# Optimization experiments

Measured on AMD Instinct MI355X. Metric: run time of the kernel, lower is better.

## Reference

```python
import jax, jax.numpy as jnp
import numpy as np

B, C, H, W = 4, 192, 56, 56
D_STATE, D_CONV, EXPAND = 16, 3, 2
D_INNER = EXPAND * C
DT_RANK = (C + 15) // 16  # 12


def setup_inputs() -> dict:
    key = jax.random.key(0)
    ks = jax.random.split(key, 16)
    s = 0.02
    return {
        "x": jax.random.normal(ks[0], (B, C, H, W), jnp.float32),
        "ln1_g": jnp.ones((C,), jnp.float32),
        "ln1_b": jnp.zeros((C,), jnp.float32),
        "in_proj_w": jax.random.normal(ks[1], (2 * D_INNER, C), jnp.float32) * s,
        "conv1d_w": jax.random.normal(ks[2], (D_INNER, 1, D_CONV), jnp.float32) * s,
        "conv1d_b": jnp.zeros((D_INNER,), jnp.float32),
        "x_proj_w": jax.random.normal(ks[3], (DT_RANK + 2 * D_STATE, D_INNER), jnp.float32) * s,
        "dt_proj_w": jax.random.normal(ks[4], (D_INNER, DT_RANK), jnp.float32) * (DT_RANK ** -0.5),
        "dt_proj_b": jax.random.uniform(ks[5], (D_INNER,), jnp.float32, -4.6, -2.3),
        "A_log": jnp.tile(jnp.log(jnp.arange(1, D_STATE + 1, dtype=jnp.float32)), (D_INNER, 1)),
        "Dskip": jnp.ones((D_INNER,), jnp.float32),
        "out_proj_w": jax.random.normal(ks[6], (C, D_INNER), jnp.float32) * s,
        "dw_w": jax.random.normal(ks[7], (C, 1, 3, 3), jnp.float32) * s,
        "bn_g": jnp.ones((C,), jnp.float32),
        "bn_b": jnp.zeros((C,), jnp.float32),
        "bn_mean": jax.random.normal(ks[8], (C,), jnp.float32) * 0.1,
        "bn_var": jax.random.uniform(ks[9], (C,), jnp.float32, 0.5, 1.5),
        "ln2_g": jnp.ones((C,), jnp.float32),
        "ln2_b": jnp.zeros((C,), jnp.float32),
        "mlp_w1": jax.random.normal(ks[10], (4 * C, C), jnp.float32) * s,
        "mlp_b1": jnp.zeros((4 * C,), jnp.float32),
        "mlp_w2": jax.random.normal(ks[11], (C, 4 * C), jnp.float32) * s,
        "mlp_b2": jnp.zeros((C,), jnp.float32),
    }


def _ln(x, g, b, eps=1e-5):
    m = jnp.mean(x, -1, keepdims=True)
    v = jnp.var(x, -1, keepdims=True)
    return (x - m) * jax.lax.rsqrt(v + eps) * g + b


def _gelu(x):
    return jax.nn.gelu(x, approximate=False)


def _mamba(xf, in_proj_w, conv1d_w, conv1d_b, x_proj_w, dt_proj_w, dt_proj_b, A_log, Dskip, out_proj_w):
    # xf: (B, L, C) tokens
    Bn, L, _ = xf.shape
    xz = jnp.einsum('blc,ec->ble', xf, in_proj_w)  # (B, L, 2*d_inner)
    xm, z = jnp.split(xz, 2, axis=-1)
    # causal depthwise conv1d over L
    xm_t = jnp.transpose(xm, (0, 2, 1))  # (B, d_inner, L)
    conv = jax.lax.conv_general_dilated(
        xm_t, conv1d_w, (1,), [(D_CONV - 1, 0)],
        feature_group_count=D_INNER,
        dimension_numbers=('NCH', 'OIH', 'NCH'))
    xm = jax.nn.silu(jnp.transpose(conv + conv1d_b[None, :, None], (0, 2, 1)))  # (B, L, d_inner)
    x_dbl = jnp.einsum('bld,ed->ble', xm, x_proj_w)
    dt = x_dbl[..., :DT_RANK]
    Bm = x_dbl[..., DT_RANK:DT_RANK + D_STATE]   # (B, L, n)
    Cm = x_dbl[..., DT_RANK + D_STATE:]          # (B, L, n)
    delta = jax.nn.softplus(jnp.einsum('blr,dr->bld', dt, dt_proj_w) + dt_proj_b)
    A = -jnp.exp(A_log)                           # (d_inner, n)
    deltaA = jnp.exp(delta[..., None] * A)        # (B, L, d, n)
    deltaBx = (delta * xm)[..., None] * Bm[:, :, None, :]  # (B, L, d, n)

    def step(h, inp):
        dA, dBx, Ct = inp
        h = dA * h + dBx                          # (B, d, n)
        y = jnp.einsum('bdn,bn->bd', h, Ct)
        return h, y

    h0 = jnp.zeros((Bn, D_INNER, D_STATE), xm.dtype)
    _, ys = jax.lax.scan(step, h0, (jnp.transpose(deltaA, (1, 0, 2, 3)),
                                    jnp.transpose(deltaBx, (1, 0, 2, 3)),
                                    jnp.transpose(Cm, (1, 0, 2))))
    y = jnp.transpose(ys, (1, 0, 2)) + xm * Dskip  # (B, L, d_inner)
    y = y * jax.nn.silu(z)
    return jnp.einsum('bld,cd->blc', y, out_proj_w)


def reference(x, ln1_g, ln1_b, in_proj_w, conv1d_w, conv1d_b, x_proj_w, dt_proj_w, dt_proj_b,
              A_log, Dskip, out_proj_w, dw_w, bn_g, bn_b, bn_mean, bn_var,
              ln2_g, ln2_b, mlp_w1, mlp_b1, mlp_w2, mlp_b2):
    Bn, Cn, Hn, Wn = x.shape
    # --- branch 1: LN -> SS2D (Mamba over flattened tokens) + skip
    t = jnp.transpose(x, (0, 2, 3, 1))            # (B, H, W, C)
    t = _ln(t, ln1_g, ln1_b)
    tokens = t.reshape(Bn, Hn * Wn, Cn)           # row-major = rearrange 'b c h w -> b (h w) c' after LN
    y = _mamba(tokens, in_proj_w, conv1d_w, conv1d_b, x_proj_w, dt_proj_w, dt_proj_b,
               A_log, Dskip, out_proj_w)
    x1 = x + jnp.transpose(y.reshape(Bn, Hn, Wn, Cn), (0, 3, 1, 2))
    # --- branch 2: depthwise conv -> BN(eval) -> GELU + skip
    dw = jax.lax.conv_general_dilated(x1, dw_w, (1, 1), [(1, 1), (1, 1)],
                                      feature_group_count=Cn,
                                      dimension_numbers=('NCHW', 'OIHW', 'NCHW'))
    bn = (dw - bn_mean[None, :, None, None]) * jax.lax.rsqrt(bn_var + 1e-5)[None, :, None, None]
    bn = bn * bn_g[None, :, None, None] + bn_b[None, :, None, None]
    x2 = x1 + _gelu(bn)
    # --- branch 3: LN -> MLP + skip
    t = jnp.transpose(x2, (0, 2, 3, 1))
    t = _ln(t, ln2_g, ln2_b)
    h = _gelu(jnp.einsum('bhwc,ec->bhwe', t, mlp_w1) + mlp_b1)
    m = jnp.einsum('bhwe,ce->bhwc', h, mlp_w2) + mlp_b2
    return x2 + jnp.transpose(m, (0, 3, 1, 2))
```

## Files before the change

kernel.cpp:

```cpp
#include <hip/hip_runtime.h>
#include <hip/hip_bf16.h>
#include <math.h>

#define BATCH 4
#define CCH   192
#define HH    56
#define WW    56
#define LSEQ  (HH*WW)
#define NTOK  (BATCH*LSEQ)
#define DST   16
#define DIN   384
#define DTR   12
#define XDM   (DTR + 2*DST)
#define CL    32
#define NC    (LSEQ/CL)

typedef __attribute__((ext_vector_type(8))) short short8;
typedef __attribute__((ext_vector_type(4))) short short4v;
typedef __attribute__((ext_vector_type(4))) float floatx4;

__device__ __forceinline__ float siluf(float x)  { return x / (1.f + __expf(-x)); }
__device__ __forceinline__ float geluf(float x)  { return 0.5f * x * (1.f + erff(x * 0.70710678118654752f)); }
__device__ __forceinline__ float softplusf(float x) { return (x > 20.f) ? x : log1pf(__expf(x)); }
__device__ __forceinline__ float bf2f(short u) {
    union { unsigned int i; float f; } cv; cv.i = ((unsigned int)(unsigned short)u) << 16; return cv.f;
}
__device__ __forceinline__ short f2bf_bits(float v) {
    __hip_bfloat16 h = __float2bfloat16(v);
    return *(short*)&h;
}

#define WSZ0 147456
#define WSZ1 16896
#define WSZ2 73728
#define WSZ3 147456
#define WSZ4 147456
__global__ __launch_bounds__(256) void cvt_weights(const float* __restrict__ w0, const float* __restrict__ w1,
                                                   const float* __restrict__ w2, const float* __restrict__ w3,
                                                   const float* __restrict__ w4,
                                                   __hip_bfloat16* __restrict__ o0, __hip_bfloat16* __restrict__ o1,
                                                   __hip_bfloat16* __restrict__ o2, __hip_bfloat16* __restrict__ o3,
                                                   __hip_bfloat16* __restrict__ o4) {
    int i = blockIdx.x * 256 + threadIdx.x;
    if (i < WSZ0) { o0[i] = __float2bfloat16(w0[i]); return; } i -= WSZ0;
    if (i < WSZ1) { o1[i] = __float2bfloat16(w1[i]); return; } i -= WSZ1;
    if (i < WSZ2) { o2[i] = __float2bfloat16(w2[i]); return; } i -= WSZ2;
    if (i < WSZ3) { o3[i] = __float2bfloat16(w3[i]); return; } i -= WSZ3;
    if (i < WSZ4) { o4[i] = __float2bfloat16(w4[i]); }
}

__global__ __launch_bounds__(256) void ln_kernel(const float* __restrict__ x,
                                                 const float* __restrict__ g,
                                                 const float* __restrict__ bta,
                                                 __hip_bfloat16* __restrict__ out) {
    __shared__ float tile[CCH * 65];
    __shared__ float gs[CCH], bs[CCH];
    int t = threadIdx.x;
    int b = blockIdx.y, hw0 = blockIdx.x * 64;
    const float* xb = x + (size_t)b * CCH * LSEQ + hw0;
#pragma unroll 8
    for (int k = 0; k < 48; k++) {
        int idx = k * 256 + t;
        int c = idx >> 6, w = idx & 63;
        tile[c * 65 + w] = xb[(size_t)c * LSEQ + w];
    }
    if (t < CCH) { gs[t] = g[t]; bs[t] = bta[t]; }
    __syncthreads();
    int lane = t & 63, wave = t >> 6;
    int tk = lane & 15, p = lane >> 4;
    int tok = wave * 16 + tk;
    float s = 0.f, s2 = 0.f;
#pragma unroll 8
    for (int i = 0; i < 48; i++) {
        float v = tile[(p * 48 + i) * 65 + tok];
        s += v; s2 += v * v;
    }
    s += __shfl_xor(s, 16); s2 += __shfl_xor(s2, 16);
    s += __shfl_xor(s, 32); s2 += __shfl_xor(s2, 32);
    float mean = s * (1.f / CCH);
    float rstd = rsqrtf(s2 * (1.f / CCH) - mean * mean + 1e-5f);
    int j = lane >> 2, q = lane & 3;
    float mj = __shfl(mean, j);
    float rj = __shfl(rstd, j);
    int wtok = wave * 16 + j;
    __hip_bfloat16* op = out + (size_t)(b * LSEQ + hw0 + wtok) * CCH + q * 48;
#pragma unroll
    for (int kk = 0; kk < 6; kk++) {
        short8 pk;
#pragma unroll
        for (int e = 0; e < 8; e++) {
            int c = q * 48 + kk * 8 + e;
            float v = (tile[c * 65 + wtok] - mj) * rj * gs[c] + bs[c];
            pk[e] = f2bf_bits(v);
        }
        *(short8*)(op + kk * 8) = pk;
    }
}

template<int EPI, typename OutT>
__global__ __launch_bounds__(256) void gemm_mfma(const __hip_bfloat16* __restrict__ A,
                                                 const __hip_bfloat16* __restrict__ W,
                                                 const float* __restrict__ bias,
                                                 const float* __restrict__ res,
                                                 OutT* __restrict__ Cout,
                                                 int N, int K) {
    __shared__ __align__(16) __hip_bfloat16 As[128 * 40];
    __shared__ __align__(16) __hip_bfloat16 Bs[128 * 40];
    int tid = threadIdx.x;
    int bm = blockIdx.y * 128, bn = blockIdx.x * 128;
    int wave = tid >> 6, lane = tid & 63;
    int wm = (wave >> 1) * 64, wn = (wave & 1) * 64;
    int lm = lane & 15, quad = lane >> 4;
    floatx4 acc[4][4] = {};
    int lrow = tid >> 2;
    int lcol = (tid & 3) * 8;
    for (int k0 = 0; k0 < K; k0 += 32) {
#pragma unroll
        for (int p = 0; p < 2; p++) {
            int row = lrow + p * 64;
            *(short8*)&As[row * 40 + lcol] = *(const short8*)(A + (size_t)(bm + row) * K + k0 + lcol);
            int n = bn + row;
            short8 bv = {0,0,0,0,0,0,0,0};
            if (n < N) bv = *(const short8*)(W + (size_t)n * K + k0 + lcol);
            *(short8*)&Bs[row * 40 + lcol] = bv;
        }
        __syncthreads();
        short8 a[4], b[4];
#pragma unroll
        for (int i = 0; i < 4; i++) a[i] = *(const short8*)&As[(wm + i * 16 + lm) * 40 + quad * 8];
#pragma unroll
        for (int j = 0; j < 4; j++) b[j] = *(const short8*)&Bs[(wn + j * 16 + lm) * 40 + quad * 8];
#pragma unroll
        for (int i = 0; i < 4; i++)
#pragma unroll
            for (int j = 0; j < 4; j++)
                acc[i][j] = __builtin_amdgcn_mfma_f32_16x16x32_bf16(a[i], b[j], acc[i][j], 0, 0, 0);
        __syncthreads();
    }
#pragma unroll
    for (int j = 0; j < 4; j++) {
        int n = bn + wn + j * 16 + lm;
        if (n >= N) continue;
        float bv = (EPI == 2 || EPI == 4) ? bias[n] : 0.f;
#pragma unroll
        for (int i = 0; i < 4; i++) {
            int mrow = bm + wm + i * 16 + quad * 4;
            if (EPI == 3 || EPI == 4) {
                int bb = mrow / LSEQ;
                int l0 = mrow % LSEQ;
                size_t oidx = ((size_t)(bb * CCH + n)) * LSEQ + l0;
                float4 xr = *(const float4*)(res + oidx);
                float4 v;
                v.x = acc[i][j][0] + bv + xr.x;
                v.y = acc[i][j][1] + bv + xr.y;
                v.z = acc[i][j][2] + bv + xr.z;
                v.w = acc[i][j][3] + bv + xr.w;
                *(float4*)((float*)Cout + oidx) = v;
            } else {
#pragma unroll
                for (int r = 0; r < 4; r++) {
                    float v = acc[i][j][r];
                    if (EPI == 2) { v += bv; v = geluf(v); }
                    Cout[(size_t)(mrow + r) * N + n] = (OutT)v;
                }
            }
        }
    }
}

__global__ __launch_bounds__(256) void gemm_nt_dt(const float* __restrict__ A,
                                                  const float* __restrict__ Wt,
                                                  const float* __restrict__ bias,
                                                  float* __restrict__ Cout) {
    __shared__ float As[16][64 + 1];
    __shared__ float Ws[16][64 + 1];
    const int N = DIN, K = DTR;
    int tid = threadIdx.x;
    int bm = blockIdx.y * 64;
    int bn = blockIdx.x * 64;
    int lr = tid >> 4;
    int lk = tid & 15;
    int tm = (tid >> 4) << 2;
    int tn = (tid & 15) << 2;
    float acc[4][4] = {};
#pragma unroll
    for (int p = 0; p < 4; p++) {
        int m = bm + lr + 16 * p;
        As[lk][lr + 16 * p] = (lk < K) ? A[(size_t)m * XDM + lk] : 0.f;
        int n = bn + lr + 16 * p;
        Ws[lk][lr + 16 * p] = (lk < K) ? Wt[(size_t)n * K + lk] : 0.f;
    }
    __syncthreads();
#pragma unroll
    for (int kk = 0; kk < 12; kk++) {
        float a[4], w[4];
#pragma unroll
        for (int i = 0; i < 4; i++) a[i] = As[kk][tm + i];
#pragma unroll
        for (int j = 0; j < 4; j++) w[j] = Ws[kk][tn + j];
#pragma unroll
        for (int i = 0; i < 4; i++)
#pragma unroll
            for (int j = 0; j < 4; j++)
                acc[i][j] += a[i] * w[j];
    }
#pragma unroll
    for (int i = 0; i < 4; i++) {
        int m = bm + tm + i;
#pragma unroll
        for (int j = 0; j < 4; j++) {
            int n = bn + tn + j;
            Cout[(size_t)m * N + n] = softplusf(acc[i][j] + bias[n]);
        }
    }
}

__global__ __launch_bounds__(256) void conv1d_silu(const __hip_bfloat16* __restrict__ xz,
                                                   const float* __restrict__ w,
                                                   const float* __restrict__ bias,
                                                   float* __restrict__ out,
                                                   __hip_bfloat16* __restrict__ out_bf) {
    int idx = blockIdx.x * 256 + threadIdx.x;
    if (idx >= NTOK * (DIN / 4)) return;
    int m = idx / (DIN / 4), d = (idx % (DIN / 4)) * 4;
    int l = m % LSEQ;
    short4v cur = *(const short4v*)&xz[(size_t)m * (2 * DIN) + d];
    short4v p1 = {0,0,0,0}, p2 = {0,0,0,0};
    if (l >= 1) p1 = *(const short4v*)&xz[(size_t)(m - 1) * (2 * DIN) + d];
    if (l >= 2) p2 = *(const short4v*)&xz[(size_t)(m - 2) * (2 * DIN) + d];
    float4 bv = *(const float4*)&bias[d];
    float ob[4];
    float4 of;
#pragma unroll
    for (int jj = 0; jj < 4; jj++) {
        float w0 = w[(d + jj) * 3 + 0], w1 = w[(d + jj) * 3 + 1], w2 = w[(d + jj) * 3 + 2];
        float acc = ((const float*)&bv)[jj] + w2 * bf2f(cur[jj]) + w1 * bf2f(p1[jj]) + w0 * bf2f(p2[jj]);
        float v = siluf(acc);
        ((float*)&of)[jj] = v;
        ob[jj] = v;
    }
    *(float4*)&out[(size_t)m * DIN + d] = of;
    short4v obv = { f2bf_bits(ob[0]), f2bf_bits(ob[1]), f2bf_bits(ob[2]), f2bf_bits(ob[3]) };
    *(short4v*)&out_bf[(size_t)m * DIN + d] = obv;
}

__global__ __launch_bounds__(256) void scan_phase1(const float* __restrict__ delta,
                                                   const float* __restrict__ xm,
                                                   const float* __restrict__ xdbl,
                                                   const float* __restrict__ A_log,
                                                   float* __restrict__ Pbuf,
                                                   float* __restrict__ Qbuf) {
    __shared__ float b_s[CL][16];
    int t = threadIdx.x;
    int b = blockIdx.z, c = blockIdx.x, d0 = blockIdx.y * 128;
    int m0 = b * LSEQ + c * CL;
    {
        int i = t >> 3, q = (t & 7) * 2;
        *(float2*)&b_s[i][q] = *(const float2*)&xdbl[(size_t)(m0 + i) * XDM + DTR + q];
    }
    __syncthreads();
    int d = d0 + (t >> 1), half = t & 1;
    float An[8];
#pragma unroll
    for (int n4 = 0; n4 < 2; n4++) {
        float4 a = *(const float4*)&A_log[d * DST + half * 8 + n4 * 4];
        An[n4 * 4 + 0] = -__expf(a.x);
        An[n4 * 4 + 1] = -__expf(a.y);
        An[n4 * 4 + 2] = -__expf(a.z);
        An[n4 * 4 + 3] = -__expf(a.w);
    }
    float Q[8];
#pragma unroll
    for (int n = 0; n < 8; n++) Q[n] = 0.f;
    float s = 0.f;
    const float* dp = delta + (size_t)m0 * DIN + d;
    const float* xp = xm    + (size_t)m0 * DIN + d;
#pragma unroll 4
    for (int i = 0; i < CL; i++) {
        float dlt = dp[(size_t)i * DIN];
        float xv  = xp[(size_t)i * DIN];
        s += dlt;
        float tt = dlt * xv;
#pragma unroll
        for (int n = 0; n < 8; n++) {
            float dA = __expf(dlt * An[n]);
            Q[n] = dA * Q[n] + tt * b_s[i][half * 8 + n];
        }
    }
    size_t o = ((size_t)(b * NC + c) * DIN + d) * DST + half * 8;
#pragma unroll
    for (int n4 = 0; n4 < 2; n4++) {
        float4 Pv, Qv;
        Pv.x = __expf(An[n4 * 4 + 0] * s);
        Pv.y = __expf(An[n4 * 4 + 1] * s);
        Pv.z = __expf(An[n4 * 4 + 2] * s);
        Pv.w = __expf(An[n4 * 4 + 3] * s);
        Qv.x = Q[n4 * 4 + 0]; Qv.y = Q[n4 * 4 + 1];
        Qv.z = Q[n4 * 4 + 2]; Qv.w = Q[n4 * 4 + 3];
        *(float4*)&Pbuf[o + n4 * 4] = Pv;
        *(float4*)&Qbuf[o + n4 * 4] = Qv;
    }
}

__global__ __launch_bounds__(256) void scan_phase2(const float* __restrict__ Pbuf,
                                                   const float* __restrict__ Qbuf,
                                                   float* __restrict__ Hin) {
    int t = blockIdx.x * 256 + threadIdx.x;
    if (t >= BATCH * DIN * DST) return;
    int b = t / (DIN * DST);
    int rem = t % (DIN * DST);
    float h = 0.f;
#pragma unroll 7
    for (int c = 0; c < NC; c++) {
        size_t o = (size_t)(b * NC + c) * (DIN * DST) + rem;
        Hin[o] = h;
        h = Pbuf[o] * h + Qbuf[o];
    }
}

__global__ __launch_bounds__(256) void scan_phase3(const float* __restrict__ delta,
                                                   const float* __restrict__ xm,
                                                   const float* __restrict__ xdbl,
                                                   const __hip_bfloat16* __restrict__ xz,
                                                   const float* __restrict__ A_log,
                                                   const float* __restrict__ Dskip,
                                                   const float* __restrict__ Hin,
                                                   __hip_bfloat16* __restrict__ ybuf) {
    __shared__ float bc_s[CL][32];
    int t = threadIdx.x;
    int b = blockIdx.z, c = blockIdx.x, d0 = blockIdx.y * 128;
    int m0 = b * LSEQ + c * CL;
    {
        int i = t >> 3, q = (t & 7) * 4;
        *(float4*)&bc_s[i][q] = *(const float4*)&xdbl[(size_t)(m0 + i) * XDM + DTR + q];
    }
    __syncthreads();
    int d = d0 + (t >> 1), half = t & 1;
    float An[8];
#pragma unroll
    for (int n4 = 0; n4 < 2; n4++) {
        float4 a = *(const float4*)&A_log[d * DST + half * 8 + n4 * 4];
        An[n4 * 4 + 0] = -__expf(a.x);
        An[n4 * 4 + 1] = -__expf(a.y);
        An[n4 * 4 + 2] = -__expf(a.z);
        An[n4 * 4 + 3] = -__expf(a.w);
    }
    float h[8];
    size_t o = ((size_t)(b * NC + c) * DIN + d) * DST + half * 8;
    {
        float4 h0 = *(const float4*)&Hin[o];
        float4 h1 = *(const float4*)&Hin[o + 4];
        h[0] = h0.x; h[1] = h0.y; h[2] = h0.z; h[3] = h0.w;
        h[4] = h1.x; h[5] = h1.y; h[6] = h1.z; h[7] = h1.w;
    }
    float Dv = Dskip[d];
    const float* dp = delta + (size_t)m0 * DIN + d;
    const float* xp = xm    + (size_t)m0 * DIN + d;
    const __hip_bfloat16* zp = xz + (size_t)m0 * (2 * DIN) + DIN + d;
    __hip_bfloat16* yo = ybuf + (size_t)m0 * DIN + d;
#pragma unroll 2
    for (int i = 0; i < CL; i++) {
        float dlt = dp[(size_t)i * DIN];
        float xv  = xp[(size_t)i * DIN];
        float tt = dlt * xv;
        float y = 0.f;
#pragma unroll
        for (int n = 0; n < 8; n++) {
            float dA = __expf(dlt * An[n]);
            h[n] = dA * h[n] + tt * bc_s[i][half * 8 + n];
            y += h[n] * bc_s[i][16 + half * 8 + n];
        }
        y += __shfl_xor(y, 1);
        if (half == 0) {
            float zv = bf2f(*(const short*)(zp + (size_t)i * (2 * DIN)));
            yo[(size_t)i * DIN] = __float2bfloat16((y + xv * Dv) * siluf(zv));
        }
    }
}

__global__ __launch_bounds__(256) void dwconv_bn_gelu(const float* __restrict__ x1,
                                                      const float* __restrict__ wdw,
                                                      const float* __restrict__ bn_g,
                                                      const float* __restrict__ bn_b,
                                                      const float* __restrict__ bn_mean,
                                                      const float* __restrict__ bn_var,
                                                      float* __restrict__ x2) {
    int idx = blockIdx.x * 256 + threadIdx.x;
    if (idx >= NTOK * CCH) return;
    int w = idx % WW; int tmp = idx / WW;
    int h = tmp % HH; tmp /= HH;
    int c = tmp % CCH; int b = tmp / CCH;
    const float* base = x1 + ((size_t)(b * CCH + c)) * LSEQ;
    float acc = 0.f;
#pragma unroll
    for (int dh = -1; dh <= 1; dh++) {
        int hh = h + dh;
        if (hh < 0 || hh >= HH) continue;
#pragma unroll
        for (int dw = -1; dw <= 1; dw++) {
            int wcol = w + dw;
            if (wcol < 0 || wcol >= WW) continue;
            acc += wdw[c * 9 + (dh + 1) * 3 + (dw + 1)] * base[hh * WW + wcol];
        }
    }
    float bn = (acc - bn_mean[c]) * rsqrtf(bn_var[c] + 1e-5f) * bn_g[c] + bn_b[c];
    x2[idx] = x1[idx] + geluf(bn);
}

extern "C" void kernel_launch(void* const* d_in, const int* in_sizes, int n_in,
                              void* d_out, int out_size, void* d_ws, size_t ws_size,
                              hipStream_t stream) {
    const float* x         = (const float*)d_in[0];
    const float* ln1_g     = (const float*)d_in[1];
    const float* ln1_b     = (const float*)d_in[2];
    const float* in_proj_w = (const float*)d_in[3];
    const float* conv_w    = (const float*)d_in[4];
    const float* conv_b    = (const float*)d_in[5];
    const float* x_proj_w  = (const float*)d_in[6];
    const float* dt_proj_w = (const float*)d_in[7];
    const float* dt_proj_b = (const float*)d_in[8];
    const float* A_log     = (const float*)d_in[9];
    const float* Dskip     = (const float*)d_in[10];
    const float* out_proj_w= (const float*)d_in[11];
    const float* dw_w      = (const float*)d_in[12];
    const float* bn_g      = (const float*)d_in[13];
    const float* bn_b      = (const float*)d_in[14];
    const float* bn_mean   = (const float*)d_in[15];
    const float* bn_var    = (const float*)d_in[16];
    const float* ln2_g     = (const float*)d_in[17];
    const float* ln2_b     = (const float*)d_in[18];
    const float* mlp_w1    = (const float*)d_in[19];
    const float* mlp_b1    = (const float*)d_in[20];
    const float* mlp_w2    = (const float*)d_in[21];
    const float* mlp_b2    = (const float*)d_in[22];
    float* out = (float*)d_out;

    float* ws = (float*)d_ws;
    __hip_bfloat16* xz_bf = (__hip_bfloat16*)ws;
    float* xm_act = (float*)(xz_bf + (size_t)NTOK * 768);
    float* deltab = xm_act + (size_t)NTOK * DIN;
    float* xdbl   = deltab + (size_t)NTOK * DIN;
    float* mo     = xdbl   + (size_t)NTOK * XDM;
    float* x1     = mo     + (size_t)NTOK * CCH;
    float* x2     = x1     + (size_t)NTOK * CCH;
    __hip_bfloat16* tokens_bf = (__hip_bfloat16*)(x2 + (size_t)NTOK * CCH);
    __hip_bfloat16* xm_bf     = tokens_bf + (size_t)NTOK * CCH;
    __hip_bfloat16* ybuf_bf   = xm_bf + (size_t)NTOK * DIN;
    __hip_bfloat16* wpool     = ybuf_bf + (size_t)NTOK * DIN;
    __hip_bfloat16* in_w_bf   = wpool;
    __hip_bfloat16* xp_w_bf   = in_w_bf + WSZ0;
    __hip_bfloat16* op_w_bf   = xp_w_bf + WSZ1;
    __hip_bfloat16* w1_bf     = op_w_bf + WSZ2;
    __hip_bfloat16* w2_bf     = w1_bf + WSZ3;
    float* Pbuf = mo;
    float* Qbuf = x1;
    float* Hin  = x2;
    __hip_bfloat16* hidden_bf = (__hip_bfloat16*)deltab;

    cvt_weights<<<(WSZ0 + WSZ1 + WSZ2 + WSZ3 + WSZ4 + 255) / 256, 256, 0, stream>>>(
        in_proj_w, x_proj_w, out_proj_w, mlp_w1, mlp_w2,
        in_w_bf, xp_w_bf, op_w_bf, w1_bf, w2_bf);
    ln_kernel<<<dim3(LSEQ / 64, BATCH), 256, 0, stream>>>(x, ln1_g, ln1_b, tokens_bf);
    gemm_mfma<0, __hip_bfloat16><<<dim3(768 / 128, NTOK / 128), 256, 0, stream>>>(tokens_bf, in_w_bf, nullptr, nullptr, xz_bf, 768, CCH);
    conv1d_silu<<<(NTOK * (DIN / 4) + 255) / 256, 256, 0, stream>>>(xz_bf, conv_w, conv_b, xm_act, xm_bf);
    gemm_mfma<0, float><<<dim3(1, NTOK / 128), 256, 0, stream>>>(xm_bf, xp_w_bf, nullptr, nullptr, xdbl, XDM, DIN);
    gemm_nt_dt<<<dim3(DIN / 64, NTOK / 64), 256, 0, stream>>>(xdbl, dt_proj_w, dt_proj_b, deltab);
    scan_phase1<<<dim3(NC, DIN / 128, BATCH), 256, 0, stream>>>(deltab, xm_act, xdbl, A_log, Pbuf, Qbuf);
    scan_phase2<<<(BATCH * DIN * DST + 255) / 256, 256, 0, stream>>>(Pbuf, Qbuf, Hin);
    scan_phase3<<<dim3(NC, DIN / 128, BATCH), 256, 0, stream>>>(deltab, xm_act, xdbl, xz_bf, A_log, Dskip, Hin, ybuf_bf);
    gemm_mfma<3, float><<<dim3(2, NTOK / 128), 256, 0, stream>>>(ybuf_bf, op_w_bf, nullptr, x, x1, CCH, DIN);
    dwconv_bn_gelu<<<(NTOK * CCH + 255) / 256, 256, 0, stream>>>(x1, dw_w, bn_g, bn_b, bn_mean, bn_var, x2);
    ln_kernel<<<dim3(LSEQ / 64, BATCH), 256, 0, stream>>>(x2, ln2_g, ln2_b, tokens_bf);
    gemm_mfma<2, __hip_bfloat16><<<dim3(768 / 128, NTOK / 128), 256, 0, stream>>>(tokens_bf, w1_bf, mlp_b1, nullptr, hidden_bf, 768, CCH);
    gemm_mfma<4, float><<<dim3(2, NTOK / 128), 256, 0, stream>>>(hidden_bf, w2_bf, mlp_b2, x2, out, CCH, 4 * CCH);
}
```

Before: 321.6 us.

## Fold dt_proj into x_proj GEMM, store scan inputs in bf16, vectorize dwconv

Precomputes a combined 416x384 weight (dt_proj_w @ x_proj_w[:12] stacked with the B/C rows), so one MFMA GEMM produces softplus(delta) in bf16 plus B/C in fp32. This removes the separate fp32 x_proj output and the small dt GEMM kernel. The scan kernels now read delta and the conv output as bf16, halving their traffic, and the fp32 copy of the conv output is dropped. The depthwise conv now handles four outputs per thread with float4 loads. The price is extra bf16 rounding on delta and the scan input, which may reduce accuracy.

```diff
diff --git a/kernel.cpp b/kernel.cpp
--- a/kernel.cpp
+++ b/kernel.cpp
@@ -12,6 +12,7 @@
 #define DIN   384
 #define DTR   12
 #define XDM   (DTR + 2*DST)
+#define NXC   416
 #define CL    32
 #define NC    (LSEQ/CL)
 
@@ -31,22 +32,37 @@
 }
 
 #define WSZ0 147456
-#define WSZ1 16896
 #define WSZ2 73728
 #define WSZ3 147456
 #define WSZ4 147456
-__global__ __launch_bounds__(256) void cvt_weights(const float* __restrict__ w0, const float* __restrict__ w1,
+__global__ __launch_bounds__(256) void cvt_weights(const float* __restrict__ w0,
                                                    const float* __restrict__ w2, const float* __restrict__ w3,
                                                    const float* __restrict__ w4,
-                                                   __hip_bfloat16* __restrict__ o0, __hip_bfloat16* __restrict__ o1,
+                                                   __hip_bfloat16* __restrict__ o0,
                                                    __hip_bfloat16* __restrict__ o2, __hip_bfloat16* __restrict__ o3,
                                                    __hip_bfloat16* __restrict__ o4) {
     int i = blockIdx.x * 256 + threadIdx.x;
     if (i < WSZ0) { o0[i] = __float2bfloat16(w0[i]); return; } i -= WSZ0;
-    if (i < WSZ1) { o1[i] = __float2bfloat16(w1[i]); return; } i -= WSZ1;
     if (i < WSZ2) { o2[i] = __float2bfloat16(w2[i]); return; } i -= WSZ2;
     if (i < WSZ3) { o3[i] = __float2bfloat16(w3[i]); return; } i -= WSZ3;
     if (i < WSZ4) { o4[i] = __float2bfloat16(w4[i]); }
+}
+
+__global__ __launch_bounds__(256) void make_wcomb(const float* __restrict__ xp_w,
+                                                  const float* __restrict__ dt_w,
+                                                  __hip_bfloat16* __restrict__ wcomb) {
+    int i = blockIdx.x * 256 + threadIdx.x;
+    if (i >= NXC * DIN) return;
+    int row = i / DIN, k = i % DIN;
+    float v;
+    if (row < DIN) {
+        v = 0.f;
+#pragma unroll
+        for (int r = 0; r < DTR; r++) v += dt_w[row * DTR + r] * xp_w[r * DIN + k];
+    } else {
+        v = xp_w[(row - DIN + DTR) * DIN + k];
+    }
+    wcomb[i] = __float2bfloat16(v);
 }
 
 __global__ __launch_bounds__(256) void ln_kernel(const float* __restrict__ x,
@@ -103,6 +119,7 @@
                                                  const float* __restrict__ bias,
                                                  const float* __restrict__ res,
                                                  OutT* __restrict__ Cout,
+                                                 float* __restrict__ aux,
                                                  int N, int K) {
     __shared__ __align__(16) __hip_bfloat16 As[128 * 40];
     __shared__ __align__(16) __hip_bfloat16 Bs[128 * 40];
@@ -141,6 +158,24 @@
     for (int j = 0; j < 4; j++) {
         int n = bn + wn + j * 16 + lm;
         if (n >= N) continue;
+        if (EPI == 5) {
+#pragma unroll
+            for (int i = 0; i < 4; i++) {
+                int mrow = bm + wm + i * 16 + quad * 4;
+                if (n < DIN) {
+                    float bv = bias[n];
+#pragma unroll
+                    for (int r = 0; r < 4; r++)
+                        Cout[(size_t)(mrow + r) * DIN + n] = (OutT)softplusf(acc[i][j][r] + bv);
+                } else {
+                    int nb = n - DIN;
+#pragma unroll
+                    for (int r = 0; r < 4; r++)
+                        aux[(size_t)(mrow + r) * 32 + nb] = acc[i][j][r];
+                }
+            }
+            continue;
+        }
         float bv = (EPI == 2 || EPI == 4) ? bias[n] : 0.f;
 #pragma unroll
         for (int i = 0; i < 4; i++) {
@@ -168,57 +203,9 @@
     }
 }
 
-__global__ __launch_bounds__(256) void gemm_nt_dt(const float* __restrict__ A,
-                                                  const float* __restrict__ Wt,
-                                                  const float* __restrict__ bias,
-                                                  float* __restrict__ Cout) {
-    __shared__ float As[16][64 + 1];
-    __shared__ float Ws[16][64 + 1];
-    const int N = DIN, K = DTR;
-    int tid = threadIdx.x;
-    int bm = blockIdx.y * 64;
-    int bn = blockIdx.x * 64;
-    int lr = tid >> 4;
-    int lk = tid & 15;
-    int tm = (tid >> 4) << 2;
-    int tn = (tid & 15) << 2;
-    float acc[4][4] = {};
-#pragma unroll
-    for (int p = 0; p < 4; p++) {
-        int m = bm + lr + 16 * p;
-        As[lk][lr + 16 * p] = (lk < K) ? A[(size_t)m * XDM + lk] : 0.f;
-        int n = bn + lr + 16 * p;
-        Ws[lk][lr + 16 * p] = (lk < K) ? Wt[(size_t)n * K + lk] : 0.f;
-    }
-    __syncthreads();
-#pragma unroll
-    for (int kk = 0; kk < 12; kk++) {
-        float a[4], w[4];
-#pragma unroll
-        for (int i = 0; i < 4; i++) a[i] = As[kk][tm + i];
-#pragma unroll
-        for (int j = 0; j < 4; j++) w[j] = Ws[kk][tn + j];
-#pragma unroll
-        for (int i = 0; i < 4; i++)
-#pragma unroll
-            for (int j = 0; j < 4; j++)
-                acc[i][j] += a[i] * w[j];
-    }
-#pragma unroll
-    for (int i = 0; i < 4; i++) {
-        int m = bm + tm + i;
-#pragma unroll
-        for (int j = 0; j < 4; j++) {
-            int n = bn + tn + j;
-            Cout[(size_t)m * N + n] = softplusf(acc[i][j] + bias[n]);
-        }
-    }
-}
-
 __global__ __launch_bounds__(256) void conv1d_silu(const __hip_bfloat16* __restrict__ xz,
                                                    const float* __restrict__ w,
                                                    const float* __restrict__ bias,
-                                                   float* __restrict__ out,
                                                    __hip_bfloat16* __restrict__ out_bf) {
     int idx = blockIdx.x * 256 + threadIdx.x;
     if (idx >= NTOK * (DIN / 4)) return;
@@ -229,24 +216,19 @@
     if (l >= 1) p1 = *(const short4v*)&xz[(size_t)(m - 1) * (2 * DIN) + d];
     if (l >= 2) p2 = *(const short4v*)&xz[(size_t)(m - 2) * (2 * DIN) + d];
     float4 bv = *(const float4*)&bias[d];
-    float ob[4];
-    float4 of;
+    short4v obv;
 #pragma unroll
     for (int jj = 0; jj < 4; jj++) {
         float w0 = w[(d + jj) * 3 + 0], w1 = w[(d + jj) * 3 + 1], w2 = w[(d + jj) * 3 + 2];
         float acc = ((const float*)&bv)[jj] + w2 * bf2f(cur[jj]) + w1 * bf2f(p1[jj]) + w0 * bf2f(p2[jj]);
-        float v = siluf(acc);
-        ((float*)&of)[jj] = v;
-        ob[jj] = v;
-    }
-    *(float4*)&out[(size_t)m * DIN + d] = of;
-    short4v obv = { f2bf_bits(ob[0]), f2bf_bits(ob[1]), f2bf_bits(ob[2]), f2bf_bits(ob[3]) };
+        obv[jj] = f2bf_bits(siluf(acc));
+    }
     *(short4v*)&out_bf[(size_t)m * DIN + d] = obv;
 }
 
-__global__ __launch_bounds__(256) void scan_phase1(const float* __restrict__ delta,
-                                                   const float* __restrict__ xm,
-                                                   const float* __restrict__ xdbl,
+__global__ __launch_bounds__(256) void scan_phase1(const __hip_bfloat16* __restrict__ delta,
+                                                   const __hip_bfloat16* __restrict__ xm,
+                                                   const float* __restrict__ bc,
                                                    const float* __restrict__ A_log,
                                                    float* __restrict__ Pbuf,
                                                    float* __restrict__ Qbuf) {
@@ -256,7 +238,7 @@
     int m0 = b * LSEQ + c * CL;
     {
         int i = t >> 3, q = (t & 7) * 2;
-        *(float2*)&b_s[i][q] = *(const float2*)&xdbl[(size_t)(m0 + i) * XDM + DTR + q];
+        *(float2*)&b_s[i][q] = *(const float2*)&bc[(size_t)(m0 + i) * 32 + q];
     }
     __syncthreads();
     int d = d0 + (t >> 1), half = t & 1;
@@ -273,12 +255,12 @@
 #pragma unroll
     for (int n = 0; n < 8; n++) Q[n] = 0.f;
     float s = 0.f;
-    const float* dp = delta + (size_t)m0 * DIN + d;
-    const float* xp = xm    + (size_t)m0 * DIN + d;
+    const __hip_bfloat16* dp = delta + (size_t)m0 * DIN + d;
+    const __hip_bfloat16* xp = xm    + (size_t)m0 * DIN + d;
 #pragma unroll 4
     for (int i = 0; i < CL; i++) {
-        float dlt = dp[(size_t)i * DIN];
-        float xv  = xp[(size_t)i * DIN];
+        float dlt = bf2f(*(const short*)(dp + (size_t)i * DIN));
+        float xv  = bf2f(*(const short*)(xp + (size_t)i * DIN));
         s += dlt;
         float tt = dlt * xv;
 #pragma unroll
@@ -318,9 +300,9 @@
     }
 }
 
-__global__ __launch_bounds__(256) void scan_phase3(const float* __restrict__ delta,
-                                                   const float* __restrict__ xm,
-                                                   const float* __restrict__ xdbl,
+__global__ __launch_bounds__(256) void scan_phase3(const __hip_bfloat16* __restrict__ delta,
+                                                   const __hip_bfloat16* __restrict__ xm,
+                                                   const float* __restrict__ bc,
                                                    const __hip_bfloat16* __restrict__ xz,
                                                    const float* __restrict__ A_log,
                                                    const float* __restrict__ Dskip,
@@ -332,7 +314,7 @@
     int m0 = b * LSEQ + c * CL;
     {
         int i = t >> 3, q = (t & 7) * 4;
-        *(float4*)&bc_s[i][q] = *(const float4*)&xdbl[(size_t)(m0 + i) * XDM + DTR + q];
+        *(float4*)&bc_s[i][q] = *(const float4*)&bc[(size_t)(m0 + i) * 32 + q];
     }
     __syncthreads();
     int d = d0 + (t >> 1), half = t & 1;
@@ -354,14 +336,14 @@
         h[4] = h1.x; h[5] = h1.y; h[6] = h1.z; h[7] = h1.w;
     }
     float Dv = Dskip[d];
-    const float* dp = delta + (size_t)m0 * DIN + d;
-    const float* xp = xm    + (size_t)m0 * DIN + d;
+    const __hip_bfloat16* dp = delta + (size_t)m0 * DIN + d;
+    const __hip_bfloat16* xp = xm    + (size_t)m0 * DIN + d;
     const __hip_bfloat16* zp = xz + (size_t)m0 * (2 * DIN) + DIN + d;
     __hip_bfloat16* yo = ybuf + (size_t)m0 * DIN + d;
 #pragma unroll 2
     for (int i = 0; i < CL; i++) {
-        float dlt = dp[(size_t)i * DIN];
-        float xv  = xp[(size_t)i * DIN];
+        float dlt = bf2f(*(const short*)(dp + (size_t)i * DIN));
+        float xv  = bf2f(*(const short*)(xp + (size_t)i * DIN));
         float tt = dlt * xv;
         float y = 0.f;
 #pragma unroll
@@ -386,25 +368,39 @@
                                                       const float* __restrict__ bn_var,
                                                       float* __restrict__ x2) {
     int idx = blockIdx.x * 256 + threadIdx.x;
-    if (idx >= NTOK * CCH) return;
-    int w = idx % WW; int tmp = idx / WW;
+    if (idx >= NTOK * CCH / 4) return;
+    int w4 = idx % (WW / 4); int tmp = idx / (WW / 4);
     int h = tmp % HH; tmp /= HH;
     int c = tmp % CCH; int b = tmp / CCH;
+    int w0 = w4 * 4;
     const float* base = x1 + ((size_t)(b * CCH + c)) * LSEQ;
-    float acc = 0.f;
+    float acc[4] = {0.f, 0.f, 0.f, 0.f};
+    float4 mid0;
 #pragma unroll
     for (int dh = -1; dh <= 1; dh++) {
         int hh = h + dh;
-        if (hh < 0 || hh >= HH) continue;
-#pragma unroll
-        for (int dw = -1; dw <= 1; dw++) {
-            int wcol = w + dw;
-            if (wcol < 0 || wcol >= WW) continue;
-            acc += wdw[c * 9 + (dh + 1) * 3 + (dw + 1)] * base[hh * WW + wcol];
-        }
-    }
-    float bn = (acc - bn_mean[c]) * rsqrtf(bn_var[c] + 1e-5f) * bn_g[c] + bn_b[c];
-    x2[idx] = x1[idx] + geluf(bn);
+        if (hh < 0 || hh >= HH) { if (dh == 0) mid0 = *(const float4*)&base[h * WW + w0]; continue; }
+        const float* row = base + hh * WW;
+        float4 mid = *(const float4*)&row[w0];
+        if (dh == 0) mid0 = mid;
+        float lft = (w0 > 0) ? row[w0 - 1] : 0.f;
+        float rgt = (w0 + 4 < WW) ? row[w0 + 4] : 0.f;
+        float wA = wdw[c * 9 + (dh + 1) * 3 + 0];
+        float wB = wdw[c * 9 + (dh + 1) * 3 + 1];
+        float wC = wdw[c * 9 + (dh + 1) * 3 + 2];
+        float in0 = lft, in1 = mid.x, in2 = mid.y, in3 = mid.z, in4 = mid.w, in5 = rgt;
+        acc[0] += wA * in0 + wB * in1 + wC * in2;
+        acc[1] += wA * in1 + wB * in2 + wC * in3;
+        acc[2] += wA * in2 + wB * in3 + wC * in4;
+        acc[3] += wA * in3 + wB * in4 + wC * in5;
+    }
+    float mu = bn_mean[c], rv = rsqrtf(bn_var[c] + 1e-5f) * bn_g[c], bb = bn_b[c];
+    float4 o;
+    o.x = mid0.x + geluf((acc[0] - mu) * rv + bb);
+    o.y = mid0.y + geluf((acc[1] - mu) * rv + bb);
+    o.z = mid0.z + geluf((acc[2] - mu) * rv + bb);
+    o.w = mid0.w + geluf((acc[3] - mu) * rv + bb);
+    *(float4*)&x2[((size_t)(b * CCH + c)) * LSEQ + h * WW + w0] = o;
 }
 
 extern "C" void kernel_launch(void* const* d_in, const int* in_sizes, int n_in,
@@ -435,42 +431,38 @@
     const float* mlp_b2    = (const float*)d_in[22];
     float* out = (float*)d_out;
 
-    float* ws = (float*)d_ws;
-    __hip_bfloat16* xz_bf = (__hip_bfloat16*)ws;
-    float* xm_act = (float*)(xz_bf + (size_t)NTOK * 768);
-    float* deltab = xm_act + (size_t)NTOK * DIN;
-    float* xdbl   = deltab + (size_t)NTOK * DIN;
-    float* mo     = xdbl   + (size_t)NTOK * XDM;
-    float* x1     = mo     + (size_t)NTOK * CCH;
-    float* x2     = x1     + (size_t)NTOK * CCH;
-    __hip_bfloat16* tokens_bf = (__hip_bfloat16*)(x2 + (size_t)NTOK * CCH);
-    __hip_bfloat16* xm_bf     = tokens_bf + (size_t)NTOK * CCH;
-    __hip_bfloat16* ybuf_bf   = xm_bf + (size_t)NTOK * DIN;
-    __hip_bfloat16* wpool     = ybuf_bf + (size_t)NTOK * DIN;
-    __hip_bfloat16* in_w_bf   = wpool;
-    __hip_bfloat16* xp_w_bf   = in_w_bf + WSZ0;
-    __hip_bfloat16* op_w_bf   = xp_w_bf + WSZ1;
-    __hip_bfloat16* w1_bf     = op_w_bf + WSZ2;
-    __hip_bfloat16* w2_bf     = w1_bf + WSZ3;
-    float* Pbuf = mo;
-    float* Qbuf = x1;
-    float* Hin  = x2;
-    __hip_bfloat16* hidden_bf = (__hip_bfloat16*)deltab;
-
-    cvt_weights<<<(WSZ0 + WSZ1 + WSZ2 + WSZ3 + WSZ4 + 255) / 256, 256, 0, stream>>>(
-        in_proj_w, x_proj_w, out_proj_w, mlp_w1, mlp_w2,
-        in_w_bf, xp_w_bf, op_w_bf, w1_bf, w2_bf);
+    char* wsb = (char*)d_ws;
+    __hip_bfloat16* xz_bf     = (__hip_bfloat16*)wsb;                 wsb += (size_t)NTOK * 768 * 2;
+    __hip_bfloat16* xm_bf     = (__hip_bfloat16*)wsb;                 wsb += (size_t)NTOK * DIN * 2;
+    __hip_bfloat16* delta_bf  = (__hip_bfloat16*)wsb;                 wsb += (size_t)NTOK * DIN * 2;
+    float*          bc        = (float*)wsb;                          wsb += (size_t)NTOK * 32 * 4;
+    float*          Pbuf      = (float*)wsb;                          wsb += (size_t)NTOK * 192 * 4;
+    float*          Qbuf      = (float*)wsb;                          wsb += (size_t)NTOK * 192 * 4;
+    float*          Hin       = (float*)wsb;                          wsb += (size_t)NTOK * 192 * 4;
+    float*          x1        = (float*)wsb;                          wsb += (size_t)NTOK * CCH * 4;
+    float*          x2        = (float*)wsb;                          wsb += (size_t)NTOK * CCH * 4;
+    __hip_bfloat16* tokens_bf = (__hip_bfloat16*)wsb;                 wsb += (size_t)NTOK * CCH * 2;
+    __hip_bfloat16* ybuf_bf   = (__hip_bfloat16*)wsb;                 wsb += (size_t)NTOK * DIN * 2;
+    __hip_bfloat16* hidden_bf = (__hip_bfloat16*)wsb;                 wsb += (size_t)NTOK * 768 * 2;
+    __hip_bfloat16* in_w_bf   = (__hip_bfloat16*)wsb;                 wsb += WSZ0 * 2;
+    __hip_bfloat16* op_w_bf   = (__hip_bfloat16*)wsb;                 wsb += WSZ2 * 2;
+    __hip_bfloat16* w1_bf     = (__hip_bfloat16*)wsb;                 wsb += WSZ3 * 2;
+    __hip_bfloat16* w2_bf     = (__hip_bfloat16*)wsb;                 wsb += WSZ4 * 2;
+    __hip_bfloat16* wcomb_bf  = (__hip_bfloat16*)wsb;                 wsb += (size_t)NXC * DIN * 2;
+
+    cvt_weights<<<(WSZ0 + WSZ2 + WSZ3 + WSZ4 + 255) / 256, 256, 0, stream>>>(
+        in_proj_w, out_proj_w, mlp_w1, mlp_w2, in_w_bf, op_w_bf, w1_bf, w2_bf);
+    make_wcomb<<<(NXC * DIN + 255) / 256, 256, 0, stream>>>(x_proj_w, dt_proj_w, wcomb_bf);
     ln_kernel<<<dim3(LSEQ / 64, BATCH), 256, 0, stream>>>(x, ln1_g, ln1_b, tokens_bf);
-    gemm_mfma<0, __hip_bfloat16><<<dim3(768 / 128, NTOK / 128), 256, 0, stream>>>(tokens_bf, in_w_bf, nullptr, nullptr, xz_bf, 768, CCH);
-    conv1d_silu<<<(NTOK * (DIN / 4) + 255) / 256, 256, 0, stream>>>(xz_bf, conv_w, conv_b, xm_act, xm_bf);
-    gemm_mfma<0, float><<<dim3(1, NTOK / 128), 256, 0, stream>>>(xm_bf, xp_w_bf, nullptr, nullptr, xdbl, XDM, DIN);
-    gemm_nt_dt<<<dim3(DIN / 64, NTOK / 64), 256, 0, stream>>>(xdbl, dt_proj_w, dt_proj_b, deltab);
-    scan_phase1<<<dim3(NC, DIN / 128, BATCH), 256, 0, stream>>>(deltab, xm_act, xdbl, A_log, Pbuf, Qbuf);
+    gemm_mfma<0, __hip_bfloat16><<<dim3(768 / 128, NTOK / 128), 256, 0, stream>>>(tokens_bf, in_w_bf, nullptr, nullptr, xz_bf, nullptr, 768, CCH);
+    conv1d_silu<<<(NTOK * (DIN / 4) + 255) / 256, 256, 0, stream>>>(xz_bf, conv_w, conv_b, xm_bf);
+    gemm_mfma<5, __hip_bfloat16><<<dim3(4, NTOK / 128), 256, 0, stream>>>(xm_bf, wcomb_bf, dt_proj_b, nullptr, delta_bf, bc, NXC, DIN);
+    scan_phase1<<<dim3(NC, DIN / 128, BATCH), 256, 0, stream>>>(delta_bf, xm_bf, bc, A_log, Pbuf, Qbuf);
     scan_phase2<<<(BATCH * DIN * DST + 255) / 256, 256, 0, stream>>>(Pbuf, Qbuf, Hin);
-    scan_phase3<<<dim3(NC, DIN / 128, BATCH), 256, 0, stream>>>(deltab, xm_act, xdbl, xz_bf, A_log, Dskip, Hin, ybuf_bf);
-    gemm_mfma<3, float><<<dim3(2, NTOK / 128), 256, 0, stream>>>(ybuf_bf, op_w_bf, nullptr, x, x1, CCH, DIN);
-    dwconv_bn_gelu<<<(NTOK * CCH + 255) / 256, 256, 0, stream>>>(x1, dw_w, bn_g, bn_b, bn_mean, bn_var, x2);
+    scan_phase3<<<dim3(NC, DIN / 128, BATCH), 256, 0, stream>>>(delta_bf, xm_bf, bc, xz_bf, A_log, Dskip, Hin, ybuf_bf);
+    gemm_mfma<3, float><<<dim3(2, NTOK / 128), 256, 0, stream>>>(ybuf_bf, op_w_bf, nullptr, x, x1, nullptr, CCH, DIN);
+    dwconv_bn_gelu<<<(NTOK * CCH / 4 + 255) / 256, 256, 0, stream>>>(x1, dw_w, bn_g, bn_b, bn_mean, bn_var, x2);
     ln_kernel<<<dim3(LSEQ / 64, BATCH), 256, 0, stream>>>(x2, ln2_g, ln2_b, tokens_bf);
-    gemm_mfma<2, __hip_bfloat16><<<dim3(768 / 128, NTOK / 128), 256, 0, stream>>>(tokens_bf, w1_bf, mlp_b1, nullptr, hidden_bf, 768, CCH);
-    gemm_mfma<4, float><<<dim3(2, NTOK / 128), 256, 0, stream>>>(hidden_bf, w2_bf, mlp_b2, x2, out, CCH, 4 * CCH);
-}
+    gemm_mfma<2, __hip_bfloat16><<<dim3(768 / 128, NTOK / 128), 256, 0, stream>>>(tokens_bf, w1_bf, mlp_b1, nullptr, hidden_bf, nullptr, 768, CCH);
+    gemm_mfma<4, float><<<dim3(2, NTOK / 128), 256, 0, stream>>>(hidden_bf, w2_bf, mlp_b2, x2, out, nullptr, CCH, 4 * CCH);
+}
```

After: 326.8 us. Within noise of the previous version (+1.6%).
